# Optimization experiments

Hardware: AMD Instinct MI355X
Metric: run time of the kernel (lower is better)

## Reference

```python
import jax, jax.numpy as jnp
import numpy as np

N_NODES = 16384
N_GRAPHS = 64
NODES_PER_GRAPH = N_NODES // N_GRAPHS
F_IN = 128
E_DIM = 256
N_HEADS = 8
MLP = 1024
N_LAYERS = 4
N_CLASSES = 10
N_EDGES = 262144
LN_EPS = 1e-5


def setup_inputs() -> dict:
    key = jax.random.key(0)
    ks = jax.random.split(key, 32)
    s = 0.02
    inp = {
        "x": jax.random.normal(ks[0], (N_NODES, F_IN), jnp.float32),
        "edge_idx": jax.random.randint(ks[1], (2, N_EDGES), 0, N_NODES, jnp.int32),
        "batch": (jnp.arange(N_NODES, dtype=jnp.int32) // NODES_PER_GRAPH),
        "pos_enc": jax.random.normal(ks[2], (N_NODES, E_DIM), jnp.float32),
        # GCNConv params (torch Linear convention: W is [out, in])
        "gcn_w": jax.random.normal(ks[3], (F_IN, F_IN), jnp.float32) * s,
        "gcn_b": jnp.zeros((F_IN,), jnp.float32),
        "cls": jax.random.normal(ks[4], (E_DIM,), jnp.float32),
        "emb_w": jax.random.normal(ks[5], (E_DIM, F_IN), jnp.float32) * s,
        "emb_b": jnp.zeros((E_DIM,), jnp.float32),
        # stacked transformer-encoder-layer params over L layers
        "in_w": jax.random.normal(ks[6], (N_LAYERS, 3 * E_DIM, E_DIM), jnp.float32) * s,
        "in_b": jnp.zeros((N_LAYERS, 3 * E_DIM), jnp.float32),
        "out_w": jax.random.normal(ks[7], (N_LAYERS, E_DIM, E_DIM), jnp.float32) * s,
        "out_b": jnp.zeros((N_LAYERS, E_DIM), jnp.float32),
        "lin1_w": jax.random.normal(ks[8], (N_LAYERS, MLP, E_DIM), jnp.float32) * s,
        "lin1_b": jnp.zeros((N_LAYERS, MLP), jnp.float32),
        "lin2_w": jax.random.normal(ks[9], (N_LAYERS, E_DIM, MLP), jnp.float32) * s,
        "lin2_b": jnp.zeros((N_LAYERS, E_DIM), jnp.float32),
        "ln1_g": jnp.ones((N_LAYERS, E_DIM), jnp.float32),
        "ln1_beta": jnp.zeros((N_LAYERS, E_DIM), jnp.float32),
        "ln2_g": jnp.ones((N_LAYERS, E_DIM), jnp.float32),
        "ln2_beta": jnp.zeros((N_LAYERS, E_DIM), jnp.float32),
        "fc_w": jax.random.normal(ks[10], (N_CLASSES, E_DIM), jnp.float32) * s,
        "fc_b": jnp.zeros((N_CLASSES,), jnp.float32),
    }
    return inp


def _layer_norm(h, g, b):
    mu = jnp.mean(h, axis=-1, keepdims=True)
    var = jnp.mean(jnp.square(h - mu), axis=-1, keepdims=True)
    return (h - mu) * jax.lax.rsqrt(var + LN_EPS) * g + b


def _gcn_conv(x, edge_idx, gcn_w, gcn_b):
    # PyG GCNConv: lin -> add self-loops -> sym-normalized scatter-add -> +bias
    xw = x @ gcn_w.T                                             # [N, F]
    ar = jnp.arange(N_NODES, dtype=edge_idx.dtype)
    ei = jnp.concatenate([edge_idx, jnp.stack([ar, ar])], axis=1)
    row, col = ei[0], ei[1]
    deg = jax.ops.segment_sum(jnp.ones(ei.shape[1], xw.dtype), col, num_segments=N_NODES)
    dinv = jax.lax.rsqrt(deg)                                    # deg >= 1 (self loops)
    norm = dinv[row] * dinv[col]                                 # [E+N]
    out = jax.ops.segment_sum(norm[:, None] * xw[row], col, num_segments=N_NODES)
    return out + gcn_b


def reference(x, edge_idx, batch, pos_enc, gcn_w, gcn_b, cls, emb_w, emb_b,
              in_w, in_b, out_w, out_b, lin1_w, lin1_b, lin2_w, lin2_b,
              ln1_g, ln1_beta, ln2_g, ln2_beta, fc_w, fc_b):
    h = _gcn_conv(x, edge_idx, gcn_w, gcn_b)
    h = jax.nn.relu(h)
    h = h @ emb_w.T + emb_b + pos_enc                            # [N, E_DIM]
    # batch = arange // NODES_PER_GRAPH (contiguous equal-size graphs):
    # per-graph loop == batched reshape
    h = h.reshape(N_GRAPHS, NODES_PER_GRAPH, E_DIM)
    cls_tok = jnp.broadcast_to(cls, (N_GRAPHS, 1, E_DIM))
    h = jnp.concatenate([cls_tok, h], axis=1)                    # [G, S, E]
    S = NODES_PER_GRAPH + 1
    dh = E_DIM // N_HEADS
    scale = 1.0 / jnp.sqrt(jnp.asarray(dh, h.dtype))
    for l in range(N_LAYERS):
        # post-LN TransformerEncoderLayer (torch default), dropout off
        qkv = jnp.einsum('gse,fe->gsf', h, in_w[l]) + in_b[l]    # [G, S, 3E]
        q, k, v = jnp.split(qkv, 3, axis=-1)
        q = q.reshape(N_GRAPHS, S, N_HEADS, dh).transpose(0, 2, 1, 3)
        k = k.reshape(N_GRAPHS, S, N_HEADS, dh).transpose(0, 2, 1, 3)
        v = v.reshape(N_GRAPHS, S, N_HEADS, dh).transpose(0, 2, 1, 3)
        att = jax.nn.softmax(jnp.einsum('ghqd,ghkd->ghqk', q, k) * scale, axis=-1)
        o = jnp.einsum('ghqk,ghkd->ghqd', att, v)
        o = o.transpose(0, 2, 1, 3).reshape(N_GRAPHS, S, E_DIM)
        o = jnp.einsum('gse,fe->gsf', o, out_w[l]) + out_b[l]
        h = _layer_norm(h + o, ln1_g[l], ln1_beta[l])
        f = jax.nn.relu(jnp.einsum('gse,me->gsm', h, lin1_w[l]) + lin1_b[l])
        f = jnp.einsum('gsm,em->gse', f, lin2_w[l]) + lin2_b[l]
        h = _layer_norm(h + f, ln2_g[l], ln2_beta[l])
    cls_out = h[:, 0, :]                                         # [G, E]
    return cls_out @ fc_w.T + fc_b                               # [G, C]
```

## Files before the change

kernel.cpp:

```cpp
#include <hip/hip_runtime.h>
#include <cstddef>

#define N_NODES 16384
#define N_GRAPHS 64
#define NPG 256
#define F_IN 128
#define E_DIM 256
#define N_HEADS 8
#define DH 32
#define MLP 1024
#define N_LAYERS 4
#define N_CLASSES 10
#define N_EDGES 262144
#define S_LEN 257
#define M_ROWS (N_GRAPHS * S_LEN)
#define M_PAD 16512
#define LN_EPS 1e-5f

typedef __attribute__((ext_vector_type(8))) short bf16x8;
typedef __attribute__((ext_vector_type(4))) float f32x4;

__device__ inline unsigned short f2b1(float f) {
    unsigned u = __float_as_uint(f);
    unsigned r = (u + 0x7fffu + ((u >> 16) & 1u)) >> 16;
    return (unsigned short)r;
}

#define GLOBAL_LOAD_LDS16(g, l) \
    __builtin_amdgcn_global_load_lds((__attribute__((address_space(1))) const void*)(g), \
                                     (__attribute__((address_space(3))) void*)(l), 16, 0, 0)

struct F2BJobs {
    const float* src[7];
    unsigned short* dst[7];
    int n4[7];
};
__global__ __launch_bounds__(256) void f2b_all(F2BJobs jobs) {
#pragma unroll 1
    for (int r = 0; r < 7; ++r) {
        const float4* s = (const float4*)jobs.src[r];
        ushort4* d = (ushort4*)jobs.dst[r];
        const int n4 = jobs.n4[r];
        for (int i = blockIdx.x * 256 + threadIdx.x; i < n4; i += gridDim.x * 256) {
            float4 v = s[i];
            ushort4 o;
            o.x = f2b1(v.x); o.y = f2b1(v.y); o.z = f2b1(v.z); o.w = f2b1(v.w);
            d[i] = o;
        }
    }
}

__global__ __launch_bounds__(256) void gemm_mfma(
    const unsigned short* __restrict__ A, const unsigned short* __restrict__ W,
    const float* __restrict__ bias, const float* __restrict__ add,
    float* __restrict__ outF, unsigned short* __restrict__ outB,
    int M, int N, int K, int relu)
{
    __shared__ __align__(16) unsigned short As0[128 * 32], As1[128 * 32];
    __shared__ __align__(16) unsigned short Bs0[128 * 32], Bs1[128 * 32];
    const int tid = threadIdx.x;
    const int wave = tid >> 6;
    const int lane = tid & 63;
    const int bm = blockIdx.y * 128;
    const int bn = blockIdx.x * 128;

    const int srow = (lane >> 2);
    const int scol = (lane & 3) * 8;
    const size_t a_r0 = (size_t)(bm + wave * 16 + srow) * K + scol;
    const size_t b_r0 = (size_t)(bn + wave * 16 + srow) * K + scol;

    const int wm = (wave & 1) * 64;
    const int wn = (wave >> 1) * 64;
    const int fr = lane & 15;
    const int fk = (lane >> 4) * 8;

    f32x4 acc[4][4];
#pragma unroll
    for (int i = 0; i < 4; ++i)
#pragma unroll
        for (int j = 0; j < 4; ++j)
            acc[i][j] = (f32x4){0.f, 0.f, 0.f, 0.f};

    auto stage = [&](unsigned short* Asb, unsigned short* Bsb, int k0) {
        GLOBAL_LOAD_LDS16(A + a_r0 + k0, Asb + wave * 512);
        GLOBAL_LOAD_LDS16(A + a_r0 + (size_t)64 * K + k0, Asb + (wave + 4) * 512);
        GLOBAL_LOAD_LDS16(W + b_r0 + k0, Bsb + wave * 512);
        GLOBAL_LOAD_LDS16(W + b_r0 + (size_t)64 * K + k0, Bsb + (wave + 4) * 512);
    };
    auto compute = [&](const unsigned short* Asb, const unsigned short* Bsb) {
        bf16x8 a[4], b[4];
#pragma unroll
        for (int i = 0; i < 4; ++i)
            a[i] = *(const bf16x8*)(Asb + (wm + i * 16 + fr) * 32 + fk);
#pragma unroll
        for (int j = 0; j < 4; ++j)
            b[j] = *(const bf16x8*)(Bsb + (wn + j * 16 + fr) * 32 + fk);
#pragma unroll
        for (int i = 0; i < 4; ++i)
#pragma unroll
            for (int j = 0; j < 4; ++j)
                acc[i][j] = __builtin_amdgcn_mfma_f32_16x16x32_bf16(a[i], b[j], acc[i][j], 0, 0, 0);
    };

    stage(As0, Bs0, 0);
    for (int k0 = 0; k0 < K; k0 += 64) {
        __syncthreads();
        if (k0 + 32 < K) stage(As1, Bs1, k0 + 32);
        compute(As0, Bs0);
        __syncthreads();
        if (k0 + 64 < K) stage(As0, Bs0, k0 + 64);
        compute(As1, Bs1);
    }

    const int er = (lane >> 4) * 4;
    const int ec = lane & 15;
#pragma unroll
    for (int j = 0; j < 4; ++j) {
        const int col = bn + wn + j * 16 + ec;
        const float bs = bias ? bias[col] : 0.f;
#pragma unroll
        for (int i = 0; i < 4; ++i) {
#pragma unroll
            for (int r = 0; r < 4; ++r) {
                const int row = bm + wm + i * 16 + er + r;
                float v = acc[i][j][r] + bs;
                if (add)  v += add[(size_t)row * N + col];
                if (relu) v = fmaxf(v, 0.f);
                if (outF) outF[(size_t)row * N + col] = v;
                if (outB) outB[(size_t)row * N + col] = f2b1(v);
            }
        }
    }
}

__global__ __launch_bounds__(256) void ln_apply(const float* __restrict__ tmp,
                                                const float* __restrict__ g,
                                                const float* __restrict__ b,
                                                float* __restrict__ h,
                                                unsigned short* __restrict__ hb) {
    __shared__ float ws1[4], ws2[4];
    __shared__ float mu_s, rstd_s;
    const int row = blockIdx.x;
    const int t = threadIdx.x;
    size_t idx = (size_t)row * E_DIM + t;
    float v = tmp[idx];
    float s1 = v, s2 = v * v;
#pragma unroll
    for (int off = 32; off > 0; off >>= 1) {
        s1 += __shfl_down(s1, off, 64);
        s2 += __shfl_down(s2, off, 64);
    }
    int wid = t >> 6, lane = t & 63;
    if (lane == 0) { ws1[wid] = s1; ws2[wid] = s2; }
    __syncthreads();
    if (t == 0) {
        float a1 = ws1[0] + ws1[1] + ws1[2] + ws1[3];
        float a2 = ws2[0] + ws2[1] + ws2[2] + ws2[3];
        float mu = a1 * (1.f / 256.f);
        float var = a2 * (1.f / 256.f) - mu * mu;
        mu_s = mu;
        rstd_s = rsqrtf(var + LN_EPS);
    }
    __syncthreads();
    float o = (v - mu_s) * rstd_s * g[t] + b[t];
    h[idx] = o;
    hb[idx] = f2b1(o);
}

__global__ void deg_count(const int* __restrict__ ei, float* __restrict__ deg) {
    int e = blockIdx.x * blockDim.x + threadIdx.x;
    if (e < N_EDGES) atomicAdd(&deg[ei[N_EDGES + e]], 1.0f);
}

__global__ __launch_bounds__(1024) void scan_deg(const float* __restrict__ deg,
                                                 int* __restrict__ row_start) {
    __shared__ int lds[1024];
    const int t = threadIdx.x;
    const int base = t * 16;
    int loc[16];
    int s = 0;
#pragma unroll
    for (int i = 0; i < 16; ++i) { loc[i] = s; s += (int)deg[base + i]; }
    lds[t] = s;
    __syncthreads();
    for (int off = 1; off < 1024; off <<= 1) {
        int v = lds[t];
        int u = (t >= off) ? lds[t - off] : 0;
        __syncthreads();
        lds[t] = v + u;
        __syncthreads();
    }
    const int excl = (t == 0) ? 0 : lds[t - 1];
#pragma unroll
    for (int i = 0; i < 16; ++i) row_start[base + i] = excl + loc[i];
    if (t == 1023) row_start[16384] = lds[1023];
}

__global__ void make_dinv(float* __restrict__ deg) {
    int i = blockIdx.x * blockDim.x + threadIdx.x;
    if (i < N_NODES) deg[i] = rsqrtf(deg[i] + 1.0f);
}

__global__ void scatter_edges(const int* __restrict__ ei, const float* __restrict__ dinv,
                              const int* __restrict__ row_start, int* __restrict__ cursor,
                              int* __restrict__ esrc, float* __restrict__ enrm) {
    int e = blockIdx.x * 256 + threadIdx.x;
    if (e < N_EDGES) {
        int r = ei[e], c = ei[N_EDGES + e];
        int slot = atomicAdd(&cursor[c], 1);
        int p = row_start[c] + slot;
        esrc[p] = r;
        enrm[p] = dinv[r] * dinv[c];
    }
}

__global__ __launch_bounds__(256) void gcn_gather(
    const float* __restrict__ xw, const int* __restrict__ row_start,
    const int* __restrict__ esrc, const float* __restrict__ enrm,
    const float* __restrict__ dinv, const float* __restrict__ bias,
    unsigned short* __restrict__ aggb) {
    const int n = blockIdx.x * 4 + (threadIdx.x >> 6);
    const int t = threadIdx.x & 63;
    const int e0 = row_start[n], e1 = row_start[n + 1];
    float ax = 0.f, ay = 0.f;
    for (int e = e0; e < e1; ++e) {
        int s = esrc[e];
        float w = enrm[e];
        float2 v = ((const float2*)(xw + (size_t)s * F_IN))[t];
        ax += w * v.x; ay += w * v.y;
    }
    const float di = dinv[n];
    const float w0 = di * di;
    float2 vs = ((const float2*)(xw + (size_t)n * F_IN))[t];
    ax += w0 * vs.x; ay += w0 * vs.y;
    float2 b2 = ((const float2*)bias)[t];
    ushort2 o;
    o.x = f2b1(fmaxf(ax + b2.x, 0.f));
    o.y = f2b1(fmaxf(ay + b2.y, 0.f));
    ((ushort2*)(aggb + (size_t)n * F_IN))[t] = o;
}

__global__ void assemble_h(const float* __restrict__ emb, const float* __restrict__ cls,
                           float* __restrict__ h, unsigned short* __restrict__ hb) {
    int row = blockIdx.x;
    int f = threadIdx.x;
    int g = row / S_LEN, s = row % S_LEN;
    float v = (s == 0) ? cls[f] : emb[((size_t)g * NPG + (s - 1)) * E_DIM + f];
    h[(size_t)row * E_DIM + f] = v;
    hb[(size_t)row * E_DIM + f] = f2b1(v);
}

__global__ __launch_bounds__(256) void attn_mfma(const unsigned short* __restrict__ qkvb,
                                                 unsigned short* __restrict__ ob) {
    const int g  = blockIdx.x >> 3;
    const int hh = blockIdx.x & 7;
    __shared__ __align__(16) unsigned short Ks[272 * 32];
    __shared__ __align__(16) unsigned short VT[32 * 288];
    __shared__ __align__(16) unsigned short Ps[4 * 16 * 288];
    const int tid  = threadIdx.x;
    const int wave = tid >> 6;
    const int lane = tid & 63;
    const int quad = lane >> 4;
    const int l16  = lane & 15;
    const size_t grow0 = (size_t)g * S_LEN;

    for (int s = tid; s < 272; s += 256) {
        uint4* dst = (uint4*)&Ks[s * 32];
        if (s < S_LEN) {
            const uint4* src = (const uint4*)(qkvb + (grow0 + s) * 768 + 256 + hh * 32);
            dst[0] = src[0]; dst[1] = src[1]; dst[2] = src[2]; dst[3] = src[3];
        } else {
            uint4 z = {0u, 0u, 0u, 0u};
            dst[0] = z; dst[1] = z; dst[2] = z; dst[3] = z;
        }
    }
    for (int s = tid; s < 288; s += 256) {
        unsigned short t[32];
        if (s < S_LEN) {
            const uint4* src = (const uint4*)(qkvb + (grow0 + s) * 768 + 512 + hh * 32);
            ((uint4*)t)[0] = src[0]; ((uint4*)t)[1] = src[1];
            ((uint4*)t)[2] = src[2]; ((uint4*)t)[3] = src[3];
        } else {
#pragma unroll
            for (int d = 0; d < 32; ++d) t[d] = 0;
        }
#pragma unroll
        for (int d = 0; d < 32; ++d) VT[d * 288 + s] = t[d];
    }
    unsigned short* Pw = &Ps[wave * 16 * 288];
    for (int i = lane; i < 256; i += 64)
        Pw[(i >> 4) * 288 + 272 + (i & 15)] = 0;
    __syncthreads();

    const float scale = 0.17677669529663687f;
    for (int qt = wave; qt < 17; qt += 4) {
        const int qrow_l = qt * 16 + l16;
        bf16x8 aq = *(const bf16x8*)(qkvb + (grow0 + qrow_l) * 768 + hh * 32 + quad * 8);

        f32x4 sc[17];
#pragma unroll
        for (int kt = 0; kt < 17; ++kt) {
            bf16x8 bk = *(const bf16x8*)&Ks[(kt * 16 + l16) * 32 + quad * 8];
            f32x4 z = (f32x4){0.f, 0.f, 0.f, 0.f};
            sc[kt] = __builtin_amdgcn_mfma_f32_16x16x32_bf16(aq, bk, z, 0, 0, 0);
        }

        float lsum[4] = {0.f, 0.f, 0.f, 0.f};
#pragma unroll
        for (int kt = 0; kt < 17; ++kt) {
#pragma unroll
            for (int r = 0; r < 4; ++r) {
                float p = __expf(sc[kt][r] * scale);
                if (kt == 16 && l16 != 0) p = 0.f;
                lsum[r] += p;
                Pw[(quad * 4 + r) * 288 + kt * 16 + l16] = f2b1(p);
            }
        }
#pragma unroll
        for (int r = 0; r < 4; ++r) {
            float s = lsum[r];
            s += __shfl_xor(s, 1, 64);
            s += __shfl_xor(s, 2, 64);
            s += __shfl_xor(s, 4, 64);
            s += __shfl_xor(s, 8, 64);
            lsum[r] = s;
        }

        f32x4 o0 = (f32x4){0.f, 0.f, 0.f, 0.f};
        f32x4 o1 = (f32x4){0.f, 0.f, 0.f, 0.f};
#pragma unroll
        for (int c = 0; c < 9; ++c) {
            bf16x8 ap  = *(const bf16x8*)&Pw[l16 * 288 + c * 32 + quad * 8];
            bf16x8 bv0 = *(const bf16x8*)&VT[l16 * 288 + c * 32 + quad * 8];
            bf16x8 bv1 = *(const bf16x8*)&VT[(16 + l16) * 288 + c * 32 + quad * 8];
            o0 = __builtin_amdgcn_mfma_f32_16x16x32_bf16(ap, bv0, o0, 0, 0, 0);
            o1 = __builtin_amdgcn_mfma_f32_16x16x32_bf16(ap, bv1, o1, 0, 0, 0);
        }

#pragma unroll
        for (int r = 0; r < 4; ++r) {
            int row_l = qt * 16 + quad * 4 + r;
            if (row_l < S_LEN) {
                float inv = 1.f / lsum[r];
                size_t orow = (grow0 + row_l) * E_DIM + hh * 32;
                ob[orow + l16]      = f2b1(o0[r] * inv);
                ob[orow + 16 + l16] = f2b1(o1[r] * inv);
            }
        }
    }
}

__global__ void fc_kernel(const float* __restrict__ h, const float* __restrict__ w,
                          const float* __restrict__ b, float* __restrict__ out) {
    int g = blockIdx.x;
    __shared__ float row[E_DIM];
    int t = threadIdx.x;
    row[t] = h[(size_t)g * S_LEN * E_DIM + t];
    __syncthreads();
    if (t < N_CLASSES) {
        float s = 0.f;
        for (int j = 0; j < E_DIM; ++j) s += row[j] * w[t * E_DIM + j];
        out[g * N_CLASSES + t] = s + b[t];
    }
}

extern "C" void kernel_launch(void* const* d_in, const int* in_sizes, int n_in,
                              void* d_out, int out_size, void* d_ws, size_t ws_size,
                              hipStream_t stream) {
    const float* x       = (const float*)d_in[0];
    const int*   edgei   = (const int*)  d_in[1];
    const float* pos_enc = (const float*)d_in[3];
    const float* gcn_w   = (const float*)d_in[4];
    const float* gcn_b   = (const float*)d_in[5];
    const float* cls     = (const float*)d_in[6];
    const float* emb_w   = (const float*)d_in[7];
    const float* emb_b   = (const float*)d_in[8];
    const float* in_w    = (const float*)d_in[9];
    const float* in_b    = (const float*)d_in[10];
    const float* out_w   = (const float*)d_in[11];
    const float* out_b   = (const float*)d_in[12];
    const float* lin1_w  = (const float*)d_in[13];
    const float* lin1_b  = (const float*)d_in[14];
    const float* lin2_w  = (const float*)d_in[15];
    const float* lin2_b  = (const float*)d_in[16];
    const float* ln1_g   = (const float*)d_in[17];
    const float* ln1_be  = (const float*)d_in[18];
    const float* ln2_g   = (const float*)d_in[19];
    const float* ln2_be  = (const float*)d_in[20];
    const float* fc_w    = (const float*)d_in[21];
    const float* fc_b    = (const float*)d_in[22];
    float* out = (float*)d_out;

    float* ws = (float*)d_ws;
    float* h    = ws;
    float* tmp  = h   + (size_t)M_PAD * E_DIM;
    float* qkv  = tmp + (size_t)M_PAD * E_DIM;
    float* xw   = qkv + (size_t)M_PAD * 768;
    float* deg  = xw  + (size_t)N_NODES * F_IN;
    int*   cursor    = (int*)(deg + N_NODES);
    int*   row_start = cursor + N_NODES;
    int*   esrc      = row_start + N_NODES + 1;
    float* enrm      = (float*)(esrc + N_EDGES);
    unsigned short* ub     = (unsigned short*)(enrm + N_EDGES);
    unsigned short* hb     = ub;
    unsigned short* attnob = hb     + (size_t)M_PAD * E_DIM;
    unsigned short* fbufb  = attnob + (size_t)M_PAD * E_DIM;
    unsigned short* xb     = fbufb  + (size_t)M_PAD * MLP;
    unsigned short* aggb   = xb     + (size_t)N_NODES * F_IN;
    unsigned short* gcn_wb = aggb   + (size_t)N_NODES * F_IN;
    unsigned short* emb_wb = gcn_wb + (size_t)F_IN * F_IN;
    unsigned short* in_wb  = emb_wb + (size_t)E_DIM * F_IN;
    unsigned short* out_wb = in_wb  + (size_t)N_LAYERS * 768 * E_DIM;
    unsigned short* lin1_wb= out_wb + (size_t)N_LAYERS * E_DIM * E_DIM;
    unsigned short* lin2_wb= lin1_wb+ (size_t)N_LAYERS * MLP * E_DIM;
    float* emb_out = qkv;
    unsigned short* qkvb = (unsigned short*)qkv;

    F2BJobs jobs;
    jobs.src[0] = x;      jobs.dst[0] = xb;      jobs.n4[0] = N_NODES * F_IN / 4;
    jobs.src[1] = gcn_w;  jobs.dst[1] = gcn_wb;  jobs.n4[1] = F_IN * F_IN / 4;
    jobs.src[2] = emb_w;  jobs.dst[2] = emb_wb;  jobs.n4[2] = E_DIM * F_IN / 4;
    jobs.src[3] = in_w;   jobs.dst[3] = in_wb;   jobs.n4[3] = N_LAYERS * 768 * E_DIM / 4;
    jobs.src[4] = out_w;  jobs.dst[4] = out_wb;  jobs.n4[4] = N_LAYERS * E_DIM * E_DIM / 4;
    jobs.src[5] = lin1_w; jobs.dst[5] = lin1_wb; jobs.n4[5] = N_LAYERS * MLP * E_DIM / 4;
    jobs.src[6] = lin2_w; jobs.dst[6] = lin2_wb; jobs.n4[6] = N_LAYERS * E_DIM * MLP / 4;
    f2b_all<<<1024, 256, 0, stream>>>(jobs);

    hipMemsetAsync(deg, 0, 2 * N_NODES * sizeof(float), stream);
    deg_count<<<(N_EDGES + 255) / 256, 256, 0, stream>>>(edgei, deg);
    scan_deg<<<1, 1024, 0, stream>>>(deg, row_start);
    make_dinv<<<(N_NODES + 255) / 256, 256, 0, stream>>>(deg);
    gemm_mfma<<<dim3(F_IN / 128, N_NODES / 128), 256, 0, stream>>>(
        xb, gcn_wb, nullptr, nullptr, xw, nullptr, N_NODES, F_IN, F_IN, 0);
    scatter_edges<<<(N_EDGES + 255) / 256, 256, 0, stream>>>(edgei, deg, row_start, cursor, esrc, enrm);
    gcn_gather<<<N_NODES / 4, 256, 0, stream>>>(xw, row_start, esrc, enrm, deg, gcn_b, aggb);

    gemm_mfma<<<dim3(E_DIM / 128, N_NODES / 128), 256, 0, stream>>>(
        aggb, emb_wb, emb_b, pos_enc, emb_out, nullptr, N_NODES, E_DIM, F_IN, 0);
    assemble_h<<<M_ROWS, E_DIM, 0, stream>>>(emb_out, cls, h, hb);

    for (int l = 0; l < N_LAYERS; ++l) {
        gemm_mfma<<<dim3(768 / 128, M_PAD / 128), 256, 0, stream>>>(
            hb, in_wb + (size_t)l * 768 * E_DIM, in_b + (size_t)l * 768, nullptr,
            nullptr, qkvb, M_PAD, 768, E_DIM, 0);
        attn_mfma<<<N_GRAPHS * N_HEADS, 256, 0, stream>>>(qkvb, attnob);
        gemm_mfma<<<dim3(E_DIM / 128, M_PAD / 128), 256, 0, stream>>>(
            attnob, out_wb + (size_t)l * E_DIM * E_DIM, out_b + (size_t)l * E_DIM, h,
            tmp, nullptr, M_PAD, E_DIM, E_DIM, 0);
        ln_apply<<<M_ROWS, E_DIM, 0, stream>>>(tmp, ln1_g + l * E_DIM, ln1_be + l * E_DIM, h, hb);
        gemm_mfma<<<dim3(MLP / 128, M_PAD / 128), 256, 0, stream>>>(
            hb, lin1_wb + (size_t)l * MLP * E_DIM, lin1_b + (size_t)l * MLP, nullptr,
            nullptr, fbufb, M_PAD, MLP, E_DIM, 1);
        gemm_mfma<<<dim3(E_DIM / 128, M_PAD / 128), 256, 0, stream>>>(
            fbufb, lin2_wb + (size_t)l * MLP * E_DIM, lin2_b + (size_t)l * E_DIM, h,
            tmp, nullptr, M_PAD, E_DIM, MLP, 0);
        ln_apply<<<M_ROWS, E_DIM, 0, stream>>>(tmp, ln2_g + l * E_DIM, ln2_be + l * E_DIM, h, hb);
    }

    fc_kernel<<<N_GRAPHS, E_DIM, 0, stream>>>(h, fc_w, fc_b, out);
}
```

Baseline: 1.046 ms.

## Split-K the N=256 projection GEMMs and fold reduction into layernorm

The attention output projection and the second MLP GEMM, both with N=256, now run as a two-way split-K kernel. This doubles the block count from 258, which is barely more than one per CU, to 516. Each split writes fp32 partials. A new ln_combine kernel adds the two partials, the bias and the residual before computing layernorm, replacing the old fused bias/residual epilogue. The cost is writing and then reading an extra fp32 partial buffer, and the tmp scratch must hold two M_PAD×256 slices.

```diff
diff --git a/kernel.cpp b/kernel.cpp
--- a/kernel.cpp
+++ b/kernel.cpp
@@ -133,17 +133,95 @@
     }
 }
 
-__global__ __launch_bounds__(256) void ln_apply(const float* __restrict__ tmp,
-                                                const float* __restrict__ g,
-                                                const float* __restrict__ b,
-                                                float* __restrict__ h,
-                                                unsigned short* __restrict__ hb) {
+__global__ __launch_bounds__(256) void gemm_splitk(
+    const unsigned short* __restrict__ A, const unsigned short* __restrict__ W,
+    float* __restrict__ part, int Kfull, int KL)
+{
+    __shared__ __align__(16) unsigned short As0[128 * 32], As1[128 * 32];
+    __shared__ __align__(16) unsigned short Bs0[128 * 32], Bs1[128 * 32];
+    const int tid = threadIdx.x;
+    const int wave = tid >> 6;
+    const int lane = tid & 63;
+    const int bm = blockIdx.y * 128;
+    const int bn = blockIdx.x * 128;
+    const int kb = blockIdx.z * KL;
+
+    const int srow = (lane >> 2);
+    const int scol = (lane & 3) * 8;
+    const size_t a_r0 = (size_t)(bm + wave * 16 + srow) * Kfull + kb + scol;
+    const size_t b_r0 = (size_t)(bn + wave * 16 + srow) * Kfull + kb + scol;
+
+    const int wm = (wave & 1) * 64;
+    const int wn = (wave >> 1) * 64;
+    const int fr = lane & 15;
+    const int fk = (lane >> 4) * 8;
+
+    f32x4 acc[4][4];
+#pragma unroll
+    for (int i = 0; i < 4; ++i)
+#pragma unroll
+        for (int j = 0; j < 4; ++j)
+            acc[i][j] = (f32x4){0.f, 0.f, 0.f, 0.f};
+
+    auto stage = [&](unsigned short* Asb, unsigned short* Bsb, int k0) {
+        GLOBAL_LOAD_LDS16(A + a_r0 + k0, Asb + wave * 512);
+        GLOBAL_LOAD_LDS16(A + a_r0 + (size_t)64 * Kfull + k0, Asb + (wave + 4) * 512);
+        GLOBAL_LOAD_LDS16(W + b_r0 + k0, Bsb + wave * 512);
+        GLOBAL_LOAD_LDS16(W + b_r0 + (size_t)64 * Kfull + k0, Bsb + (wave + 4) * 512);
+    };
+    auto compute = [&](const unsigned short* Asb, const unsigned short* Bsb) {
+        bf16x8 a[4], b[4];
+#pragma unroll
+        for (int i = 0; i < 4; ++i)
+            a[i] = *(const bf16x8*)(Asb + (wm + i * 16 + fr) * 32 + fk);
+#pragma unroll
+        for (int j = 0; j < 4; ++j)
+            b[j] = *(const bf16x8*)(Bsb + (wn + j * 16 + fr) * 32 + fk);
+#pragma unroll
+        for (int i = 0; i < 4; ++i)
+#pragma unroll
+            for (int j = 0; j < 4; ++j)
+                acc[i][j] = __builtin_amdgcn_mfma_f32_16x16x32_bf16(a[i], b[j], acc[i][j], 0, 0, 0);
+    };
+
+    stage(As0, Bs0, 0);
+    for (int k0 = 0; k0 < KL; k0 += 64) {
+        __syncthreads();
+        if (k0 + 32 < KL) stage(As1, Bs1, k0 + 32);
+        compute(As0, Bs0);
+        __syncthreads();
+        if (k0 + 64 < KL) stage(As0, Bs0, k0 + 64);
+        compute(As1, Bs1);
+    }
+
+    float* p = part + (size_t)blockIdx.z * M_PAD * 256;
+    const int er = (lane >> 4) * 4;
+    const int ec = lane & 15;
+#pragma unroll
+    for (int j = 0; j < 4; ++j) {
+        const int col = bn + wn + j * 16 + ec;
+#pragma unroll
+        for (int i = 0; i < 4; ++i)
+#pragma unroll
+            for (int r = 0; r < 4; ++r) {
+                const int row = bm + wm + i * 16 + er + r;
+                p[(size_t)row * 256 + col] = acc[i][j][r];
+            }
+    }
+}
+
+__global__ __launch_bounds__(256) void ln_combine(const float* __restrict__ part,
+                                                  const float* __restrict__ bias,
+                                                  const float* __restrict__ g,
+                                                  const float* __restrict__ b,
+                                                  float* __restrict__ h,
+                                                  unsigned short* __restrict__ hb) {
     __shared__ float ws1[4], ws2[4];
     __shared__ float mu_s, rstd_s;
     const int row = blockIdx.x;
     const int t = threadIdx.x;
     size_t idx = (size_t)row * E_DIM + t;
-    float v = tmp[idx];
+    float v = part[idx] + part[(size_t)M_PAD * 256 + idx] + bias[t] + h[idx];
     float s1 = v, s2 = v * v;
 #pragma unroll
     for (int off = 32; off > 0; off >>= 1) {
@@ -415,6 +493,7 @@
     unsigned short* lin2_wb= lin1_wb+ (size_t)N_LAYERS * MLP * E_DIM;
     float* emb_out = qkv;
     unsigned short* qkvb = (unsigned short*)qkv;
+    float* part = tmp;
 
     F2BJobs jobs;
     jobs.src[0] = x;      jobs.dst[0] = xb;      jobs.n4[0] = N_NODES * F_IN / 4;
@@ -444,17 +523,17 @@
             hb, in_wb + (size_t)l * 768 * E_DIM, in_b + (size_t)l * 768, nullptr,
             nullptr, qkvb, M_PAD, 768, E_DIM, 0);
         attn_mfma<<<N_GRAPHS * N_HEADS, 256, 0, stream>>>(qkvb, attnob);
-        gemm_mfma<<<dim3(E_DIM / 128, M_PAD / 128), 256, 0, stream>>>(
-            attnob, out_wb + (size_t)l * E_DIM * E_DIM, out_b + (size_t)l * E_DIM, h,
-            tmp, nullptr, M_PAD, E_DIM, E_DIM, 0);
-        ln_apply<<<M_ROWS, E_DIM, 0, stream>>>(tmp, ln1_g + l * E_DIM, ln1_be + l * E_DIM, h, hb);
+        gemm_splitk<<<dim3(2, M_PAD / 128, 2), 256, 0, stream>>>(
+            attnob, out_wb + (size_t)l * E_DIM * E_DIM, part, E_DIM, E_DIM / 2);
+        ln_combine<<<M_ROWS, E_DIM, 0, stream>>>(
+            part, out_b + (size_t)l * E_DIM, ln1_g + l * E_DIM, ln1_be + l * E_DIM, h, hb);
         gemm_mfma<<<dim3(MLP / 128, M_PAD / 128), 256, 0, stream>>>(
             hb, lin1_wb + (size_t)l * MLP * E_DIM, lin1_b + (size_t)l * MLP, nullptr,
             nullptr, fbufb, M_PAD, MLP, E_DIM, 1);
-        gemm_mfma<<<dim3(E_DIM / 128, M_PAD / 128), 256, 0, stream>>>(
-            fbufb, lin2_wb + (size_t)l * MLP * E_DIM, lin2_b + (size_t)l * E_DIM, h,
-            tmp, nullptr, M_PAD, E_DIM, MLP, 0);
-        ln_apply<<<M_ROWS, E_DIM, 0, stream>>>(tmp, ln2_g + l * E_DIM, ln2_be + l * E_DIM, h, hb);
+        gemm_splitk<<<dim3(2, M_PAD / 128, 2), 256, 0, stream>>>(
+            fbufb, lin2_wb + (size_t)l * MLP * E_DIM, part, MLP, MLP / 2);
+        ln_combine<<<M_ROWS, E_DIM, 0, stream>>>(
+            part, lin2_b + (size_t)l * E_DIM, ln2_g + l * E_DIM, ln2_be + l * E_DIM, h, hb);
     }
 
     fc_kernel<<<N_GRAPHS, E_DIM, 0, stream>>>(h, fc_w, fc_b, out);
```

Result: faster. 928.5 us (-11.2%).
